# Optimization experiments

Measured on AMD Instinct MI355X. Metric: run time of the kernel, lower is better.

Reference implementation:

```python
import jax, jax.numpy as jnp
import numpy as np

# Straight-through sign binarization (BinaryNet semantics: .data mutation => identity grad)
@jax.custom_vjp
def binarize(x):
    return jnp.sign(x)

def _bin_fwd(x):
    return jnp.sign(x), None

def _bin_bwd(res, g):
    return (g,)

binarize.defvjp(_bin_fwd, _bin_bwd)

def hardtanh(x):
    return jnp.clip(x, -1.0, 1.0)

def bconv2d(x, w, stride):
    # binarize both input and weight, VALID conv, NCHW/OIHW
    return jax.lax.conv_general_dilated(
        binarize(x), binarize(w),
        window_strides=(stride, stride), padding='VALID',
        dimension_numbers=('NCHW', 'OIHW', 'NCHW'))

def blinear(x, w):
    # binarize input and weight; w is [out, in]
    return binarize(x) @ binarize(w).T

def setup_inputs() -> dict:
    key = jax.random.key(0)
    ks = jax.random.split(key, 6)
    B = 131072
    return {
        'x':    jax.random.normal(ks[0], (B, 1, 15, 15), dtype=jnp.float32),
        'w1':   jax.random.normal(ks[1], (4, 1, 3, 3),  dtype=jnp.float32),
        'w2':   jax.random.normal(ks[2], (8, 4, 3, 3),  dtype=jnp.float32),
        'w3':   jax.random.normal(ks[3], (16, 8, 3, 3), dtype=jnp.float32),
        'wfc1': jax.random.normal(ks[4], (8, 16),       dtype=jnp.float32),
        'wfc2': jax.random.normal(ks[5], (1, 8),        dtype=jnp.float32),
    }

def reference(x, w1, w2, w3, wfc1, wfc2):
    out = hardtanh(bconv2d(x, w1, 2))        # [B,4,7,7]
    out = hardtanh(bconv2d(out, w2, 2))      # [B,8,3,3]
    out = hardtanh(bconv2d(out, w3, 2))      # [B,16,1,1]
    out = out.reshape(-1, 16)                # [B,16]
    out = hardtanh(blinear(out, wfc1))       # [B,8]
    out = blinear(out, wfc2)                 # [B,1]
    return out
```

## Files before the change

kernel.cpp:

```cpp
#include <hip/hip_runtime.h>
#include <stdint.h>

typedef uint32_t u32;
typedef uint64_t u64;


__global__ void prep_weights(const float* __restrict__ w1, const float* __restrict__ w2,
                             const float* __restrict__ w3, const float* __restrict__ wfc1,
                             const float* __restrict__ wfc2, u32* __restrict__ ws) {
  const int tid = threadIdx.x;
  if (tid < 81) ws[tid] = 0;
  __syncthreads();
  for (int i = tid; i < 1612; i += 1024) {
    if (i < 36) {
      const int c = i / 9, k = i % 9;
      if (w1[i] < 0.f) atomicOr(&ws[c], 1u << k);
    } else if (i < 324) {
      const int j = i - 36, d = j / 36, r = j % 36;
      const int c = r / 9, t = r % 9, ky = t / 3, kx = t % 3;
      const int bp = 12 * ky + 4 * kx + c;
      if (w2[j] < 0.f) atomicOr(&ws[8 + 2 * d + (bp >> 5)], 1u << (bp & 31));
    } else if (i < 1476) {
      const int j = i - 324, e = j / 72, r = j % 72;
      const int d = r / 9, t = r % 9, ky = t / 3, kx = t % 3;
      const int bp = 8 * (3 * ky + kx) + d;
      if (w3[j] < 0.f) {
        if (bp < 64) atomicOr(&ws[24 + 2 * e + (bp >> 5)], 1u << (bp & 31));
        else         atomicOr(&ws[56 + e], 1u << (bp - 64));
      }
    } else if (i < 1604) {
      const int j = i - 1476, row = j / 16, e = j % 16;
      if (wfc1[j] < 0.f) atomicOr(&ws[72 + row], 1u << e);
    } else {
      const int j = i - 1604;
      if (wfc2[j] < 0.f) atomicOr(&ws[80], 1u << j);
    }
  }
}

__global__ __launch_bounds__(256) void binnet(const float* __restrict__ x,
                                              const u32* __restrict__ ws,
                                              float* __restrict__ out) {
  __shared__ u64 st[4][228];
  const int tid = threadIdx.x;
  const int wv = tid >> 6, lane = tid & 63;
  const int b = blockIdx.x;

  const float* xw = x + (size_t)(b * 256 + wv * 64) * 225 + lane;
  if (lane < 3) st[wv][225 + lane] = 0;
  #pragma unroll
  for (int g = 0; g < 5; ++g) {
    float v[45];
    #pragma unroll
    for (int k = 0; k < 45; ++k) v[k] = xw[(g * 45 + k) * 64];
    #pragma unroll
    for (int k = 0; k < 45; ++k) {
      const u64 m = __ballot(v[k] < 0.f);
      if (lane == 0) st[wv][g * 45 + k] = m;
    }
  }
  __syncthreads();

  const u64* stw = st[wv];
  const int f0 = 225 * lane;
  const int w0 = f0 >> 6;
  const int sh = f0 & 63;
  u64 Wd[5];
  #pragma unroll
  for (int i = 0; i < 5; ++i) Wd[i] = stw[w0 + i];
  u64 Bv[4];
  #pragma unroll
  for (int i = 0; i < 4; ++i)
    Bv[i] = (Wd[i] >> sh) | ((Wd[i + 1] << (63 - sh)) << 1);

  u32 rb[15];
  #pragma unroll
  for (int r = 0; r < 15; ++r) {
    const int f = 15 * r, w = f >> 6, o = f & 63;
    u64 v = Bv[w] >> o;
    if (o > 49) v |= Bv[w + 1] << (64 - o);
    rb[r] = (u32)v & 0x7FFFu;
  }

  const u32 w1p0 = ws[0], w1p1 = ws[1], w1p2 = ws[2], w1p3 = ws[3];
  u64 a1[4] = {0, 0, 0, 0};
  int pix = 0;
  #pragma unroll
  for (int oy = 0; oy < 7; ++oy) {
    const u32 r0 = rb[2 * oy], r1 = rb[2 * oy + 1], r2 = rb[2 * oy + 2];
    #pragma unroll
    for (int ox = 0; ox < 7; ++ox) {
      const u32 t9 = ((r0 >> (2 * ox)) & 7) | (((r1 >> (2 * ox)) & 7) << 3)
                   | (((r2 >> (2 * ox)) & 7) << 6);
      u32 nib = 0;
      nib |= (u32)(__popc(t9 ^ w1p0) >= 5) << 0;
      nib |= (u32)(__popc(t9 ^ w1p1) >= 5) << 1;
      nib |= (u32)(__popc(t9 ^ w1p2) >= 5) << 2;
      nib |= (u32)(__popc(t9 ^ w1p3) >= 5) << 3;
      a1[pix >> 4] |= (u64)nib << ((pix & 15) * 4);
      ++pix;
    }
  }

  const u64* w2qp = (const u64*)(ws + 8);
  u64 W2[8];
  #pragma unroll
  for (int d = 0; d < 8; ++d) W2[d] = w2qp[d];
  u64 v2lo = 0, nz2lo = 0; u32 v2hi = 0, nz2hi = 0;
  #pragma unroll
  for (int oy = 0; oy < 3; ++oy) {
    #pragma unroll
    for (int ox = 0; ox < 3; ++ox) {
      u64 T = 0;
      #pragma unroll
      for (int ky = 0; ky < 3; ++ky) {
        const int p = 4 * (7 * (2 * oy + ky) + 2 * ox);
        const int w = p >> 6, o = p & 63;
        u64 v = a1[w] >> o;
        if (o > 52) v |= a1[w + 1] << (64 - o);
        T |= (v & 0xFFFull) << (12 * ky);
      }
      const int pix2 = 3 * oy + ox;
      u32 bv = 0, bz = 0;
      #pragma unroll
      for (int d = 0; d < 8; ++d) {
        const int cnt = __popcll(T ^ W2[d]);
        bv |= (u32)(cnt > 18) << d;
        bz |= (u32)(cnt != 18) << d;
      }
      if (pix2 < 8) { v2lo |= (u64)bv << (8 * pix2); nz2lo |= (u64)bz << (8 * pix2); }
      else          { v2hi = bv; nz2hi = bz; }
    }
  }

  const u64* w3lo = (const u64*)(ws + 24);
  const u32* w3hi = ws + 56;
  u64 W3L[16]; u32 W3H[16];
  #pragma unroll
  for (int e = 0; e < 16; ++e) { W3L[e] = w3lo[e]; W3H[e] = w3hi[e]; }
  const int nztot = __popcll(nz2lo) + __popc(nz2hi);
  u32 s3v = 0, s3nz = 0;
  #pragma unroll
  for (int e = 0; e < 16; ++e) {
    const int cnt = __popcll(nz2lo & (v2lo ^ W3L[e])) + __popc(nz2hi & (v2hi ^ W3H[e]));
    const int s = nztot - 2 * cnt;
    s3v  |= (u32)(s < 0) << e;
    s3nz |= (u32)(s != 0) << e;
  }

  const u32* wf1 = ws + 72;
  u32 WF1[8];
  #pragma unroll
  for (int j = 0; j < 8; ++j) WF1[j] = wf1[j];
  const int n3 = __popc(s3nz);
  u32 hv = 0, hz = 0;
  #pragma unroll
  for (int j = 0; j < 8; ++j) {
    const int c2 = __popc(s3nz & (s3v ^ WF1[j]));
    const int s = n3 - 2 * c2;
    hv |= (u32)(s < 0) << j;
    hz |= (u32)(s != 0) << j;
  }

  const u32 wf2 = ws[80];
  const int c3 = __popc(hz & (hv ^ wf2));
  const int sfin = __popc(hz) - 2 * c3;
  out[b * 256 + wv * 64 + lane] = (float)sfin;
}

extern "C" void kernel_launch(void* const* d_in, const int* in_sizes, int n_in,
                              void* d_out, int out_size, void* d_ws, size_t ws_size,
                              hipStream_t stream) {
  const float* x    = (const float*)d_in[0];
  const float* w1   = (const float*)d_in[1];
  const float* w2   = (const float*)d_in[2];
  const float* w3   = (const float*)d_in[3];
  const float* wfc1 = (const float*)d_in[4];
  const float* wfc2 = (const float*)d_in[5];
  u32* ws = (u32*)d_ws;
  float* out = (float*)d_out;
  const int B = in_sizes[0] / 225;

  prep_weights<<<1, 1024, 0, stream>>>(w1, w2, w3, wfc1, wfc2, ws);
  binnet<<<B / 256, 256, 0, stream>>>(x, ws, out);
}
```

Before: 189.6 us.

## Stage input tiles via global_load_lds DMA and extract sign bits from LDS

Drops the per-element register loads and per-element wave ballots used to pack input signs. The block now copies each wave's contiguous 57.6 KB input chunk straight into LDS with 16-byte global_load_lds transfers, then the owning wave reads its lane's 225 floats and packs the sign bits directly into its bitfield. The aim is fewer load and ballot instructions and no cross-lane bit realignment. In exchange, the four chunks are processed in sequence with two barriers each, only one wave computes per phase, and the large LDS footprint limits how many blocks fit on a CU. Taking the raw sign bit also treats -0.0 as negative, unlike the previous `v < 0` test.

After: 189.6 us. About the same (+0.0%).

```diff
diff --git a/kernel.cpp b/kernel.cpp
--- a/kernel.cpp
+++ b/kernel.cpp
@@ -38,40 +38,50 @@
   }
 }
 
+__device__ __forceinline__ void gload_lds16(const void* g, void* l) {
+  __builtin_amdgcn_global_load_lds(
+      (const __attribute__((address_space(1))) void*)g,
+      (__attribute__((address_space(3))) void*)l, 16, 0, 0);
+}
+__device__ __forceinline__ void gload_lds4(const void* g, void* l) {
+  __builtin_amdgcn_global_load_lds(
+      (const __attribute__((address_space(1))) void*)g,
+      (__attribute__((address_space(3))) void*)l, 4, 0, 0);
+}
+
 __global__ __launch_bounds__(256) void binnet(const float* __restrict__ x,
                                               const u32* __restrict__ ws,
                                               float* __restrict__ out) {
-  __shared__ u64 st[4][228];
+  __shared__ __align__(16) float stage[14400];
   const int tid = threadIdx.x;
   const int wv = tid >> 6, lane = tid & 63;
   const int b = blockIdx.x;
 
-  const float* xw = x + (size_t)(b * 256 + wv * 64) * 225 + lane;
-  if (lane < 3) st[wv][225 + lane] = 0;
-  #pragma unroll
-  for (int g = 0; g < 5; ++g) {
-    float v[45];
-    #pragma unroll
-    for (int k = 0; k < 45; ++k) v[k] = xw[(g * 45 + k) * 64];
-    #pragma unroll
-    for (int k = 0; k < 45; ++k) {
-      const u64 m = __ballot(v[k] < 0.f);
-      if (lane == 0) st[wv][g * 45 + k] = m;
+  u64 Bv[4] = {0, 0, 0, 0};
+  const char* xb = (const char*)x + (size_t)b * 230400;
+
+  #pragma unroll 1
+  for (int p = 0; p < 4; ++p) {
+    const char* gbase = xb + p * 57600;
+    if (wv == 0) gload_lds4(gbase + 57344 + lane * 4, (char*)stage + 57344 + lane * 4);
+    for (int j = wv; j < 56; j += 4)
+      gload_lds16(gbase + j * 1024 + lane * 16, (char*)stage + j * 1024 + lane * 16);
+    __syncthreads();
+
+    if (wv == p) {
+      const float* myf = stage + 225 * lane;
+      #pragma unroll
+      for (int k = 0; k < 56; ++k) {
+        const u32 n = (__float_as_uint(myf[4 * k + 0]) >> 31)
+                    | ((__float_as_uint(myf[4 * k + 1]) >> 31) << 1)
+                    | ((__float_as_uint(myf[4 * k + 2]) >> 31) << 2)
+                    | ((__float_as_uint(myf[4 * k + 3]) >> 31) << 3);
+        Bv[k >> 4] |= (u64)n << ((4 * k) & 63);
+      }
+      Bv[3] |= (u64)(__float_as_uint(myf[224]) >> 31) << 32;
     }
+    __syncthreads();
   }
-  __syncthreads();
-
-  const u64* stw = st[wv];
-  const int f0 = 225 * lane;
-  const int w0 = f0 >> 6;
-  const int sh = f0 & 63;
-  u64 Wd[5];
-  #pragma unroll
-  for (int i = 0; i < 5; ++i) Wd[i] = stw[w0 + i];
-  u64 Bv[4];
-  #pragma unroll
-  for (int i = 0; i < 4; ++i)
-    Bv[i] = (Wd[i] >> sh) | ((Wd[i + 1] << (63 - sh)) << 1);
 
   u32 rb[15];
   #pragma unroll
```
